# Performance work log

Hardware: AMD Instinct MI355X
Metric: run time of the kernel (lower is better)

Reference implementation:

```python
import jax, jax.numpy as jnp
import numpy as np

B, C, N = 8, 64, 4096

def setup_inputs() -> dict:
    key = jax.random.key(0)
    k1, k2, k3 = jax.random.split(key, 3)
    k = jax.random.normal(k1, (B, C, N), dtype=jnp.float32)
    q = jax.random.normal(k2, (B, C, N), dtype=jnp.float32)
    v = jax.random.normal(k3, (B, C, N), dtype=jnpp.float32) if False else jax.random.normal(k3, (B, C, N), dtype=jnp.float32)
    return {"k": k, "q": q, "v": v}

def reference(k, q, v):
    input_dim = k.shape[1]  # C
    # similarity = k^T @ q : [B, N, N]
    scores = jnp.einsum('bcn,bcm->bnm', k, q) / jnp.sqrt(jnp.float32(input_dim))
    attn = jax.nn.softmax(scores, axis=-1)  # softmax over last dim (query positions m)
    # out = attn @ v^T : [B, N, C], then transpose back to [B, C, N]
    out = jnp.einsum('bnm,bcm->bcn', attn, v)
    return out
```

## Files before the change

kernel.cpp:

```cpp
#include <hip/hip_runtime.h>
#include <stdint.h>

typedef __attribute__((ext_vector_type(8)))  __bf16        bf16x8;
typedef __attribute__((ext_vector_type(8)))  unsigned short u16x8;
typedef __attribute__((ext_vector_type(4)))  float          f32x4;
typedef __attribute__((ext_vector_type(16))) float          f32x16;
typedef __attribute__((ext_vector_type(4)))  unsigned int   u32x4;

#define NB 8
#define NC 64
#define NN 4096
#define NCHUNK 64
#define CHUNK_U16 4096
#define SPLITQ 4

#define EXP2F(x) __builtin_amdgcn_exp2f(x)

__device__ __forceinline__ unsigned short f2bf(float x) {
    unsigned int u = __builtin_bit_cast(unsigned int, x);
    u += 0x7fffu + ((u >> 16) & 1u);
    return (unsigned short)(u >> 16);
}
__device__ __forceinline__ unsigned int pk2(float a, float b) {
    unsigned short x = __builtin_bit_cast(unsigned short, (__bf16)a);
    unsigned short y = __builtin_bit_cast(unsigned short, (__bf16)b);
    return (unsigned int)x | ((unsigned int)y << 16);
}

__global__ __launch_bounds__(256) void prepass(
    const float* __restrict__ qp, const float* __restrict__ vp,
    unsigned short* __restrict__ qfo, unsigned short* __restrict__ vfo)
{
    __shared__ float lt[64][68];
    const int orig = blockIdx.x;
    const int bid = (orig & 7) * 64 + (orig >> 3);
    const int b = bid >> 6, mc = bid & 63;
    const int m0 = mc * 64;
    const int tid = threadIdx.x;
    const float* qb = qp + (size_t)b * NC * NN;
    const float* vb = vp + (size_t)b * NC * NN;
    unsigned short* qfc = qfo + (size_t)bid * CHUNK_U16;
    unsigned short* vfc = vfo + (size_t)bid * CHUNK_U16;

    #pragma unroll
    for (int rep = 0; rep < 4; ++rep) {
        int idx = tid + 256 * rep;
        int c = idx >> 4, m4 = (idx & 15) << 2;
        f32x4 xv = *reinterpret_cast<const f32x4*>(qb + (size_t)c * NN + m0 + m4);
        lt[m4+0][c] = xv[0]; lt[m4+1][c] = xv[1];
        lt[m4+2][c] = xv[2]; lt[m4+3][c] = xv[3];
    }
    __syncthreads();
    #pragma unroll
    for (int rep = 0; rep < 2; ++rep) {
        int fid = tid + 256 * rep;
        int l = fid & 63, kk = (fid >> 6) & 3, mt = fid >> 8;
        int m = 32 * mt + (l & 31), c0 = 16 * kk + 8 * (l >> 5);
        u16x8 ov;
        #pragma unroll
        for (int e = 0; e < 8; ++e) ov[e] = f2bf(lt[m][c0 + e]);
        *reinterpret_cast<u16x8*>(qfc + (size_t)fid * 8) = ov;
    }
    __syncthreads();
    #pragma unroll
    for (int rep = 0; rep < 4; ++rep) {
        int idx = tid + 256 * rep;
        int c = idx >> 4, m4 = (idx & 15) << 2;
        f32x4 xv = *reinterpret_cast<const f32x4*>(vb + (size_t)c * NN + m0 + m4);
        *reinterpret_cast<f32x4*>(&lt[c][m4]) = xv;
    }
    __syncthreads();
    #pragma unroll
    for (int rep = 0; rep < 2; ++rep) {
        int fid = tid + 256 * rep;
        int l = fid & 63, kt = (fid >> 6) & 3, ct = fid >> 8;
        int c = 32 * ct + (l & 31), mm = 16 * kt + 8 * (l >> 5);
        u16x8 ov;
        #pragma unroll
        for (int e = 0; e < 8; ++e) ov[e] = f2bf(lt[c][mm + e]);
        *reinterpret_cast<u16x8*>(vfc + (size_t)fid * 8) = ov;
    }
}

template<int SPLITQ_T>
__global__ __launch_bounds__(64, 3) void attn13(
    const float* __restrict__ kp,
    const unsigned short* __restrict__ qfo,
    const unsigned short* __restrict__ vfo,
    float* __restrict__ part, float* __restrict__ lp)
{
    constexpr int CPQ_T = NCHUNK / SPLITQ_T;
    constexpr int NT32 = NN / 32;
    constexpr int PER_XCD = SPLITQ_T * NT32;

    const int orig = blockIdx.x;
    const int bid  = (orig & 7) * PER_XCD + (orig >> 3);
    const int b    = bid / PER_XCD;
    const int rest = bid % PER_XCD;
    const int qid  = rest / NT32;
    const int t32  = rest % NT32;
    const int n0 = t32 * 32;
    const int l = threadIdx.x;
    const int lo5 = l & 31, hi = l >> 5;
    const int nrow = n0 + lo5;

    switch (orig & 3) {
        case 1: __builtin_amdgcn_s_sleep(5);  break;
        case 2: __builtin_amdgcn_s_sleep(10); break;
        case 3: __builtin_amdgcn_s_sleep(15); break;
        default: break;
    }

    const float kscale = 0.125f * 1.44269504088896f;
    const float* kb = kp + (size_t)b * NC * NN;
    bf16x8 kf[4];
    #pragma unroll
    for (int kk = 0; kk < 4; ++kk) {
        u16x8 t;
        #pragma unroll
        for (int e = 0; e < 8; ++e)
            t[e] = __builtin_bit_cast(unsigned short,
                      (__bf16)(kscale * kb[(size_t)(16 * kk + 8 * hi + e) * NN + nrow]));
        kf[kk] = __builtin_bit_cast(bf16x8, t);
    }

    const unsigned short* qg = qfo + (size_t)(b * NCHUNK + qid * CPQ_T) * CHUNK_U16;
    const unsigned short* vg = vfo + (size_t)(b * NCHUNK + qid * CPQ_T) * CHUNK_U16;

    f32x16 zro;
    #pragma unroll
    for (int r = 0; r < 16; ++r) zro[r] = 0.f;
    f32x16 o0 = zro, o1 = zro;
    float sum = 0.f;

    u16x8 a[8], vf[8];
    #pragma unroll
    for (int f = 0; f < 8; ++f)
        a[f] = *reinterpret_cast<const u16x8*>(qg + (f * 64 + l) * 8);
    #pragma unroll
    for (int f = 0; f < 8; ++f)
        vf[f] = *reinterpret_cast<const u16x8*>(vg + (f * 64 + l) * 8);

    for (int mcr = 0; mcr < CPQ_T; ++mcr) {
        __builtin_amdgcn_s_setprio(1);
        f32x16 s0 = __builtin_amdgcn_mfma_f32_32x32x16_bf16(__builtin_bit_cast(bf16x8, a[0]), kf[0], zro, 0, 0, 0);
        f32x16 s1 = __builtin_amdgcn_mfma_f32_32x32x16_bf16(__builtin_bit_cast(bf16x8, a[4]), kf[0], zro, 0, 0, 0);
        #pragma unroll
        for (int kk = 1; kk < 4; ++kk) {
            s0 = __builtin_amdgcn_mfma_f32_32x32x16_bf16(__builtin_bit_cast(bf16x8, a[kk]),     kf[kk], s0, 0, 0, 0);
            s1 = __builtin_amdgcn_mfma_f32_32x32x16_bf16(__builtin_bit_cast(bf16x8, a[4 + kk]), kf[kk], s1, 0, 0, 0);
        }
        __builtin_amdgcn_s_setprio(0);

        if (mcr + 1 < CPQ_T) {
            const unsigned short* qn = qg + (size_t)(mcr + 1) * CHUNK_U16;
            #pragma unroll
            for (int f = 0; f < 8; ++f)
                a[f] = *reinterpret_cast<const u16x8*>(qn + (f * 64 + l) * 8);
        }

        float ps0 = 0.f, ps1 = 0.f, ps2 = 0.f, ps3 = 0.f;
        #pragma unroll
        for (int r = 0; r < 16; r += 4) {
            s0[r]   = EXP2F(s0[r]);   ps0 += s0[r];
            s0[r+1] = EXP2F(s0[r+1]); ps1 += s0[r+1];
            s0[r+2] = EXP2F(s0[r+2]); ps2 += s0[r+2];
            s0[r+3] = EXP2F(s0[r+3]); ps3 += s0[r+3];
        }
        #pragma unroll
        for (int r = 0; r < 16; r += 4) {
            s1[r]   = EXP2F(s1[r]);   ps0 += s1[r];
            s1[r+1] = EXP2F(s1[r+1]); ps1 += s1[r+1];
            s1[r+2] = EXP2F(s1[r+2]); ps2 += s1[r+2];
            s1[r+3] = EXP2F(s1[r+3]); ps3 += s1[r+3];
        }
        sum += (ps0 + ps1) + (ps2 + ps3);

        #pragma unroll
        for (int kt = 0; kt < 4; ++kt) {
            const f32x16& sm = (kt < 2) ? s0 : s1;
            const int qA = 2 * (kt & 1);
            unsigned int w0 = pk2(sm[4*qA+0], sm[4*qA+1]);
            unsigned int w1 = pk2(sm[4*qA+2], sm[4*qA+3]);
            unsigned int w2 = pk2(sm[4*qA+4], sm[4*qA+5]);
            unsigned int w3 = pk2(sm[4*qA+6], sm[4*qA+7]);
            asm volatile("v_permlane32_swap_b32 %0, %1" : "+v"(w0), "+v"(w2));
            asm volatile("v_permlane32_swap_b32 %0, %1" : "+v"(w1), "+v"(w3));
            u32x4 pf = (u32x4){w0, w1, w2, w3};
            bf16x8 pB = __builtin_bit_cast(bf16x8, pf);
            __builtin_amdgcn_s_setprio(1);
            o0 = __builtin_amdgcn_mfma_f32_32x32x16_bf16(__builtin_bit_cast(bf16x8, vf[kt]),     pB, o0, 0, 0, 0);
            o1 = __builtin_amdgcn_mfma_f32_32x32x16_bf16(__builtin_bit_cast(bf16x8, vf[4 + kt]), pB, o1, 0, 0, 0);
            __builtin_amdgcn_s_setprio(0);
        }

        if (mcr + 1 < CPQ_T) {
            const unsigned short* vn = vg + (size_t)(mcr + 1) * CHUNK_U16;
            #pragma unroll
            for (int f = 0; f < 8; ++f)
                vf[f] = *reinterpret_cast<const u16x8*>(vn + (f * 64 + l) * 8);
        }
    }

    sum += (float)__shfl_xor(sum, 32);
    const int t64 = t32 >> 1;
    const int rowoff = 32 * (t32 & 1);
    const int pidx = (b * 64 + t64) * SPLITQ_T + qid;
    float* po = part + (size_t)pidx * 4096;
    #pragma unroll
    for (int r = 0; r < 16; ++r) {
        int cb = (r & 3) + 8 * (r >> 2) + 4 * hi;
        po[cb * 64 + rowoff + lo5]        = o0[r];
        po[(32 + cb) * 64 + rowoff + lo5] = o1[r];
    }
    if (hi == 0) lp[(size_t)pidx * 64 + rowoff + lo5] = sum;
}

__global__ __launch_bounds__(256) void combine2(
    const float* __restrict__ part, const float* __restrict__ lp,
    float* __restrict__ outp, int splitq)
{
    __shared__ float sinv[64];
    const int orig = blockIdx.x;
    const int bid = (orig & 7) * 64 + (orig >> 3);
    const int b = bid >> 6, tile = bid & 63;
    const int n0 = tile * 64;
    const int t = threadIdx.x;
    const int pb = bid * splitq;

    if (t < 64) {
        float L = 0.f;
        for (int q = 0; q < splitq; ++q) L += lp[(size_t)(pb + q) * 64 + t];
        sinv[t] = 1.0f / L;
    }
    __syncthreads();

    float* ob = outp + (size_t)b * NC * NN;
    #pragma unroll
    for (int it = 0; it < 4; ++it) {
        int idx = it * 1024 + t * 4;
        int ch = idx >> 6, r0 = idx & 63;
        f32x4 acc = (f32x4){0.f, 0.f, 0.f, 0.f};
        for (int q = 0; q < splitq; ++q) {
            f32x4 v = *reinterpret_cast<const f32x4*>(part + (size_t)(pb + q) * 4096 + idx);
            acc += v;
        }
        f32x4 res;
        #pragma unroll
        for (int u = 0; u < 4; ++u) res[u] = acc[u] * sinv[r0 + u];
        *reinterpret_cast<f32x4*>(ob + (size_t)ch * NN + n0 + r0) = res;
    }
}

__global__ __launch_bounds__(128) void attn2(
    const float* __restrict__ kp,
    const unsigned short* __restrict__ qfo,
    const unsigned short* __restrict__ vfo,
    float* __restrict__ outp)
{
    __shared__ unsigned short sb[2][2 * CHUNK_U16];
    const int orig = blockIdx.x;
    const int bid  = (orig & 7) * 64 + (orig >> 3);
    const int b = bid >> 6, nt = bid & 63;
    const int n0 = nt * 64;
    const int tid = threadIdx.x;
    const int w = tid >> 6, l = tid & 63;
    const int lo5 = l & 31, hi = l >> 5;
    const int nrow = n0 + 32 * w + lo5;
    const float kscale = 0.125f * 1.44269504088896f;
    const float* kb = kp + (size_t)b * NC * NN;
    bf16x8 kf[4];
    #pragma unroll
    for (int kk = 0; kk < 4; ++kk) {
        u16x8 t;
        #pragma unroll
        for (int e = 0; e < 8; ++e)
            t[e] = f2bf(kscale * kb[(size_t)(16 * kk + 8 * hi + e) * NN + nrow]);
        kf[kk] = __builtin_bit_cast(bf16x8, t);
    }
    const unsigned short* qg = qfo + (size_t)(b * 64) * CHUNK_U16;
    const unsigned short* vg = vfo + (size_t)(b * 64) * CHUNK_U16;
    auto stage = [&](int mc, int buf) {
        const unsigned short* gq = qg + (size_t)mc * CHUNK_U16;
        const unsigned short* gv = vg + (size_t)mc * CHUNK_U16;
        #pragma unroll
        for (int i = 0; i < 4; ++i) {
            int seg = w * 4 + i;
            int off = seg * 512 + l * 8;
            __builtin_amdgcn_global_load_lds(
                (const __attribute__((address_space(1))) void*)(gq + off),
                (__attribute__((address_space(3))) void*)(&sb[buf][seg * 512]), 16, 0, 0);
            __builtin_amdgcn_global_load_lds(
                (const __attribute__((address_space(1))) void*)(gv + off),
                (__attribute__((address_space(3))) void*)(&sb[buf][CHUNK_U16 + seg * 512]), 16, 0, 0);
        }
    };
    stage(0, 0);
    __syncthreads();
    f32x16 o0, o1;
    #pragma unroll
    for (int r = 0; r < 16; ++r) { o0[r] = 0.f; o1[r] = 0.f; }
    float m_run = -1e30f, l_run = 0.f;
    for (int mc = 0; mc < NCHUNK; ++mc) {
        const int cur = mc & 1;
        if (mc + 1 < NCHUNK) stage(mc + 1, cur ^ 1);
        const unsigned short* qb_ = &sb[cur][0];
        const unsigned short* vb_ = &sb[cur][CHUNK_U16];
        f32x16 s0, s1;
        #pragma unroll
        for (int r = 0; r < 16; ++r) { s0[r] = 0.f; s1[r] = 0.f; }
        #pragma unroll
        for (int kk = 0; kk < 4; ++kk) {
            u16x8 a0 = *reinterpret_cast<const u16x8*>(qb_ + ((0 * 4 + kk) * 64 + l) * 8);
            u16x8 a1 = *reinterpret_cast<const u16x8*>(qb_ + ((1 * 4 + kk) * 64 + l) * 8);
            s0 = __builtin_amdgcn_mfma_f32_32x32x16_bf16(__builtin_bit_cast(bf16x8, a0), kf[kk], s0, 0, 0, 0);
            s1 = __builtin_amdgcn_mfma_f32_32x32x16_bf16(__builtin_bit_cast(bf16x8, a1), kf[kk], s1, 0, 0, 0);
        }
        float pmax = s0[0];
        #pragma unroll
        for (int r = 1; r < 16; ++r) pmax = fmaxf(pmax, s0[r]);
        #pragma unroll
        for (int r = 0; r < 16; ++r) pmax = fmaxf(pmax, s1[r]);
        pmax = fmaxf(pmax, (float)__shfl_xor(pmax, 32));
        const float mn = fmaxf(m_run, pmax);
        const float alpha = EXP2F(m_run - mn);
        float sum = 0.f;
        #pragma unroll
        for (int r = 0; r < 16; ++r) { s0[r] = EXP2F(s0[r] - mn); sum += s0[r]; }
        #pragma unroll
        for (int r = 0; r < 16; ++r) { s1[r] = EXP2F(s1[r] - mn); sum += s1[r]; }
        sum += (float)__shfl_xor(sum, 32);
        l_run = l_run * alpha + sum;
        m_run = mn;
        #pragma unroll
        for (int r = 0; r < 16; ++r) { o0[r] *= alpha; o1[r] *= alpha; }
        #pragma unroll
        for (int kt = 0; kt < 4; ++kt) {
            const f32x16& sm = (kt < 2) ? s0 : s1;
            const int qA = 2 * (kt & 1);
            unsigned int dA0 = pk2(sm[4 * qA + 0], sm[4 * qA + 1]);
            unsigned int dA1 = pk2(sm[4 * qA + 2], sm[4 * qA + 3]);
            unsigned int dB0 = pk2(sm[4 * qA + 4], sm[4 * qA + 5]);
            unsigned int dB1 = pk2(sm[4 * qA + 6], sm[4 * qA + 7]);
            unsigned int sA0 = (unsigned int)__shfl_xor((int)dA0, 32);
            unsigned int sA1 = (unsigned int)__shfl_xor((int)dA1, 32);
            unsigned int sB0 = (unsigned int)__shfl_xor((int)dB0, 32);
            unsigned int sB1 = (unsigned int)__shfl_xor((int)dB1, 32);
            u32x4 pf;
            if (hi == 0) pf = (u32x4){dA0, dA1, sA0, sA1};
            else         pf = (u32x4){sB0, sB1, dB0, dB1};
            bf16x8 pB = __builtin_bit_cast(bf16x8, pf);
            u16x8 v0 = *reinterpret_cast<const u16x8*>(vb_ + ((0 * 4 + kt) * 64 + l) * 8);
            u16x8 v1 = *reinterpret_cast<const u16x8*>(vb_ + ((1 * 4 + kt) * 64 + l) * 8);
            o0 = __builtin_amdgcn_mfma_f32_32x32x16_bf16(__builtin_bit_cast(bf16x8, v0), pB, o0, 0, 0, 0);
            o1 = __builtin_amdgcn_mfma_f32_32x32x16_bf16(__builtin_bit_cast(bf16x8, v1), pB, o1, 0, 0, 0);
        }
        __syncthreads();
    }
    const float inv = 1.0f / l_run;
    float* ob = outp + (size_t)b * NC * NN;
    #pragma unroll
    for (int r = 0; r < 16; ++r) {
        int cb = (r & 3) + 8 * (r >> 2) + 4 * hi;
        ob[(size_t)cb * NN + n0 + 32 * w + lo5]        = o0[r] * inv;
        ob[(size_t)(32 + cb) * NN + n0 + 32 * w + lo5] = o1[r] * inv;
    }
}

__global__ __launch_bounds__(256) void attn_fwd(
    const float* __restrict__ kp, const float* __restrict__ qp,
    const float* __restrict__ vp, float* __restrict__ outp)
{
    __shared__ unsigned short qs[8][64][8];
    __shared__ unsigned short vs[8][64][8];
    __shared__ unsigned short ps[4][2][64][8];
    const int orig = blockIdx.x;
    const int bid  = (orig & 7) * 64 + (orig >> 3);
    const int b  = bid >> 6;
    const int n0 = (bid & 63) * 64;
    const int tid = threadIdx.x;
    const int w = tid >> 6, l = tid & 63, g = l >> 4, j = l & 15;
    const float* kb = kp + (size_t)b * NC * NN;
    const float* qb = qp + (size_t)b * NC * NN;
    const float* vb = vp + (size_t)b * NC * NN;
    bf16x8 ak[2];
    #pragma unroll
    for (int kk = 0; kk < 2; ++kk) {
        u16x8 tmp;
        #pragma unroll
        for (int e = 0; e < 8; ++e)
            tmp[e] = f2bf(kb[(size_t)(32*kk + 8*g + e) * NN + (n0 + 16*w + j)]);
        ak[kk] = __builtin_bit_cast(bf16x8, tmp);
    }
    f32x4 o[4];
    float m_run[4], l_run[4];
    #pragma unroll
    for (int ct = 0; ct < 4; ++ct) o[ct] = (f32x4){0.f,0.f,0.f,0.f};
    #pragma unroll
    for (int r = 0; r < 4; ++r) { m_run[r] = -1e30f; l_run[r] = 0.0f; }
    for (int m0 = 0; m0 < NN; m0 += 64) {
        __syncthreads();
        #pragma unroll
        for (int it = 0; it < 4; ++it) {
            int f = tid + 256*it;
            int c = f >> 4, m4 = (f & 15) << 2;
            f32x4 qv = *reinterpret_cast<const f32x4*>(qb + (size_t)c*NN + m0 + m4);
            f32x4 vv = *reinterpret_cast<const f32x4*>(vb + (size_t)c*NN + m0 + m4);
            int kkq = c >> 5, eq = c & 7, gq = (c >> 3) & 3, tq = m4 >> 4;
            #pragma unroll
            for (int u = 0; u < 4; ++u)
                qs[kkq*4 + tq][16*gq + ((m4 + u) & 15)][eq] = f2bf(qv[u]);
            int ctv = c >> 4, jv = c & 15, kkv = m4 >> 5, gv = (m4 >> 3) & 3, ev = m4 & 7;
            #pragma unroll
            for (int u = 0; u < 4; ++u)
                vs[kkv*4 + ctv][16*gv + jv][ev + u] = f2bf(vv[u]);
        }
        __syncthreads();
        f32x4 s[4];
        #pragma unroll
        for (int t = 0; t < 4; ++t) {
            f32x4 acc = (f32x4){0.f,0.f,0.f,0.f};
            #pragma unroll
            for (int kk = 0; kk < 2; ++kk) {
                u16x8 raw = *reinterpret_cast<const u16x8*>(&qs[kk*4 + t][l][0]);
                acc = __builtin_amdgcn_mfma_f32_16x16x32_bf16(ak[kk], __builtin_bit_cast(bf16x8, raw), acc, 0,0,0);
            }
            s[t] = acc * 0.125f;
        }
        float alpha[4];
        #pragma unroll
        for (int r = 0; r < 4; ++r) {
            float m1 = fmaxf(fmaxf(s[0][r], s[1][r]), fmaxf(s[2][r], s[3][r]));
            #pragma unroll
            for (int off = 1; off < 16; off <<= 1) m1 = fmaxf(m1, __shfl_xor(m1, off));
            float mn = fmaxf(m_run[r], m1);
            alpha[r] = __expf(m_run[r] - mn);
            m_run[r] = mn;
            float acc = 0.0f;
            #pragma unroll
            for (int t = 0; t < 4; ++t) { float p = __expf(s[t][r] - mn); s[t][r] = p; acc += p; }
            #pragma unroll
            for (int off = 1; off < 16; off <<= 1) acc += __shfl_xor(acc, off);
            l_run[r] = l_run[r] * alpha[r] + acc;
        }
        {
            int srcl = (j >> 2) << 4;
            float a0 = __shfl(alpha[0], srcl), a1 = __shfl(alpha[1], srcl);
            float a2 = __shfl(alpha[2], srcl), a3 = __shfl(alpha[3], srcl);
            int rs = j & 3;
            float ac = (rs==0)?a0:(rs==1)?a1:(rs==2)?a2:a3;
            #pragma unroll
            for (int ct = 0; ct < 4; ++ct) o[ct] *= ac;
        }
        #pragma unroll
        for (int t = 0; t < 4; ++t) {
            int m = 16*t + j;
            #pragma unroll
            for (int r = 0; r < 4; ++r)
                ps[w][m >> 5][((m >> 3) & 3)*16 + 4*g + r][m & 7] = f2bf(s[t][r]);
        }
        asm volatile("s_waitcnt lgkmcnt(0)" ::: "memory");
        #pragma unroll
        for (int kk2 = 0; kk2 < 2; ++kk2) {
            u16x8 rp = *reinterpret_cast<const u16x8*>(&ps[w][kk2][l][0]);
            bf16x8 bp = __builtin_bit_cast(bf16x8, rp);
            #pragma unroll
            for (int ct = 0; ct < 4; ++ct) {
                u16x8 rv = *reinterpret_cast<const u16x8*>(&vs[kk2*4 + ct][l][0]);
                o[ct] = __builtin_amdgcn_mfma_f32_16x16x32_bf16(__builtin_bit_cast(bf16x8, rv), bp, o[ct], 0,0,0);
            }
        }
    }
    {
        int srcl = (j >> 2) << 4;
        float l0 = __shfl(l_run[0], srcl), l1 = __shfl(l_run[1], srcl);
        float l2 = __shfl(l_run[2], srcl), l3 = __shfl(l_run[3], srcl);
        int rs = j & 3;
        float lc = (rs==0)?l0:(rs==1)?l1:(rs==2)?l2:l3;
        float inv = 1.0f / lc;
        #pragma unroll
        for (int ct = 0; ct < 4; ++ct)
            #pragma unroll
            for (int r = 0; r < 4; ++r)
                outp[(size_t)b*NC*NN + (size_t)(16*ct + 4*g + r)*NN + (n0 + 16*w + j)] = o[ct][r] * inv;
    }
}

extern "C" void kernel_launch(void* const* d_in, const int* in_sizes, int n_in,
                              void* d_out, int out_size, void* d_ws, size_t ws_size,
                              hipStream_t stream) {
    const float* kp = (const float*)d_in[0];
    const float* qp = (const float*)d_in[1];
    const float* vp = (const float*)d_in[2];
    float* op = (float*)d_out;
    const size_t FRAG_BYTES = (size_t)2 * NB * NCHUNK * CHUNK_U16 * sizeof(unsigned short);
    unsigned short* qfo = (unsigned short*)d_ws;
    unsigned short* vfo = qfo + (size_t)NB * NCHUNK * CHUNK_U16;

    const size_t NEED = FRAG_BYTES
        + (size_t)NB * 64 * SPLITQ * 4096 * sizeof(float)
        + (size_t)NB * 64 * SPLITQ * 64 * sizeof(float);

    if (ws_size >= NEED) {
        float* part = (float*)((char*)d_ws + FRAG_BYTES);
        float* lpp  = part + (size_t)NB * 64 * SPLITQ * 4096;
        hipLaunchKernelGGL(prepass, dim3(NB * NCHUNK), dim3(256), 0, stream, qp, vp, qfo, vfo);
        hipLaunchKernelGGL(attn13<SPLITQ>, dim3(NB * SPLITQ * (NN / 32)), dim3(64), 0, stream,
                           kp, qfo, vfo, part, lpp);
        hipLaunchKernelGGL(combine2, dim3(NB * 64), dim3(256), 0, stream, part, lpp, op, SPLITQ);
    } else if (ws_size >= FRAG_BYTES) {
        hipLaunchKernelGGL(prepass, dim3(NB * NCHUNK), dim3(256), 0, stream, qp, vp, qfo, vfo);
        hipLaunchKernelGGL(attn2, dim3(NB * NCHUNK), dim3(128), 0, stream, kp, qfo, vfo, op);
    } else {
        hipLaunchKernelGGL(attn_fwd, dim3(512), dim3(256), 0, stream, kp, qp, vp, op);
    }
}
```

Baseline: 70.21 us.

## Software-pipeline QK MFMA of next chunk with softmax of current chunk

Restructures the attention loop into a two-stage ping-pong: the QK^T MFMAs for chunk i+1 are issued while the exp and pack work for chunk i runs, with Q loads moved two chunks ahead. The goal is to overlap matrix-core latency with the VALU exponentials instead of running them back to back. It also drops the staggered s_sleep start, removes the setprio hints, and lowers the launch-bounds occupancy hint from 3 to 2 to leave room for the extra live score registers. Fewer waves per SIMD may reduce latency hiding across waves.

```diff
diff --git a/kernel.cpp b/kernel.cpp
--- a/kernel.cpp
+++ b/kernel.cpp
@@ -83,7 +83,7 @@
 }
 
 template<int SPLITQ_T>
-__global__ __launch_bounds__(64, 3) void attn13(
+__global__ __launch_bounds__(64, 2) void attn15(
     const float* __restrict__ kp,
     const unsigned short* __restrict__ qfo,
     const unsigned short* __restrict__ vfo,
@@ -104,13 +104,6 @@
     const int lo5 = l & 31, hi = l >> 5;
     const int nrow = n0 + lo5;
 
-    switch (orig & 3) {
-        case 1: __builtin_amdgcn_s_sleep(5);  break;
-        case 2: __builtin_amdgcn_s_sleep(10); break;
-        case 3: __builtin_amdgcn_s_sleep(15); break;
-        default: break;
-    }
-
     const float kscale = 0.125f * 1.44269504088896f;
     const float* kb = kp + (size_t)b * NC * NN;
     bf16x8 kf[4];
@@ -141,44 +134,40 @@
     for (int f = 0; f < 8; ++f)
         vf[f] = *reinterpret_cast<const u16x8*>(vg + (f * 64 + l) * 8);
 
-    for (int mcr = 0; mcr < CPQ_T; ++mcr) {
-        __builtin_amdgcn_s_setprio(1);
-        f32x16 s0 = __builtin_amdgcn_mfma_f32_32x32x16_bf16(__builtin_bit_cast(bf16x8, a[0]), kf[0], zro, 0, 0, 0);
-        f32x16 s1 = __builtin_amdgcn_mfma_f32_32x32x16_bf16(__builtin_bit_cast(bf16x8, a[4]), kf[0], zro, 0, 0, 0);
-        #pragma unroll
-        for (int kk = 1; kk < 4; ++kk) {
-            s0 = __builtin_amdgcn_mfma_f32_32x32x16_bf16(__builtin_bit_cast(bf16x8, a[kk]),     kf[kk], s0, 0, 0, 0);
-            s1 = __builtin_amdgcn_mfma_f32_32x32x16_bf16(__builtin_bit_cast(bf16x8, a[4 + kk]), kf[kk], s1, 0, 0, 0);
-        }
-        __builtin_amdgcn_s_setprio(0);
-
-        if (mcr + 1 < CPQ_T) {
-            const unsigned short* qn = qg + (size_t)(mcr + 1) * CHUNK_U16;
-            #pragma unroll
-            for (int f = 0; f < 8; ++f)
-                a[f] = *reinterpret_cast<const u16x8*>(qn + (f * 64 + l) * 8);
-        }
-
+    f32x16 sA0, sA1, sB0, sB1;
+    sA0 = __builtin_amdgcn_mfma_f32_32x32x16_bf16(__builtin_bit_cast(bf16x8, a[0]), kf[0], zro, 0, 0, 0);
+    sA1 = __builtin_amdgcn_mfma_f32_32x32x16_bf16(__builtin_bit_cast(bf16x8, a[4]), kf[0], zro, 0, 0, 0);
+    #pragma unroll
+    for (int kk = 1; kk < 4; ++kk) {
+        sA0 = __builtin_amdgcn_mfma_f32_32x32x16_bf16(__builtin_bit_cast(bf16x8, a[kk]),     kf[kk], sA0, 0, 0, 0);
+        sA1 = __builtin_amdgcn_mfma_f32_32x32x16_bf16(__builtin_bit_cast(bf16x8, a[4 + kk]), kf[kk], sA1, 0, 0, 0);
+    }
+    #pragma unroll
+    for (int f = 0; f < 8; ++f)
+        a[f] = *reinterpret_cast<const u16x8*>(qg + CHUNK_U16 + (f * 64 + l) * 8);
+
+    auto phase = [&](f32x16& c0, f32x16& c1, f32x16& nx0, f32x16& nx1, int idx) {
         float ps0 = 0.f, ps1 = 0.f, ps2 = 0.f, ps3 = 0.f;
         #pragma unroll
         for (int r = 0; r < 16; r += 4) {
-            s0[r]   = EXP2F(s0[r]);   ps0 += s0[r];
-            s0[r+1] = EXP2F(s0[r+1]); ps1 += s0[r+1];
-            s0[r+2] = EXP2F(s0[r+2]); ps2 += s0[r+2];
-            s0[r+3] = EXP2F(s0[r+3]); ps3 += s0[r+3];
+            c0[r]   = EXP2F(c0[r]);   ps0 += c0[r];
+            c0[r+1] = EXP2F(c0[r+1]); ps1 += c0[r+1];
+            c0[r+2] = EXP2F(c0[r+2]); ps2 += c0[r+2];
+            c0[r+3] = EXP2F(c0[r+3]); ps3 += c0[r+3];
         }
         #pragma unroll
         for (int r = 0; r < 16; r += 4) {
-            s1[r]   = EXP2F(s1[r]);   ps0 += s1[r];
-            s1[r+1] = EXP2F(s1[r+1]); ps1 += s1[r+1];
-            s1[r+2] = EXP2F(s1[r+2]); ps2 += s1[r+2];
-            s1[r+3] = EXP2F(s1[r+3]); ps3 += s1[r+3];
+            c1[r]   = EXP2F(c1[r]);   ps0 += c1[r];
+            c1[r+1] = EXP2F(c1[r+1]); ps1 += c1[r+1];
+            c1[r+2] = EXP2F(c1[r+2]); ps2 += c1[r+2];
+            c1[r+3] = EXP2F(c1[r+3]); ps3 += c1[r+3];
         }
         sum += (ps0 + ps1) + (ps2 + ps3);
 
+        bf16x8 pB[4];
         #pragma unroll
         for (int kt = 0; kt < 4; ++kt) {
-            const f32x16& sm = (kt < 2) ? s0 : s1;
+            const f32x16& sm = (kt < 2) ? c0 : c1;
             const int qA = 2 * (kt & 1);
             unsigned int w0 = pk2(sm[4*qA+0], sm[4*qA+1]);
             unsigned int w1 = pk2(sm[4*qA+2], sm[4*qA+3]);
@@ -187,19 +176,41 @@
             asm volatile("v_permlane32_swap_b32 %0, %1" : "+v"(w0), "+v"(w2));
             asm volatile("v_permlane32_swap_b32 %0, %1" : "+v"(w1), "+v"(w3));
             u32x4 pf = (u32x4){w0, w1, w2, w3};
-            bf16x8 pB = __builtin_bit_cast(bf16x8, pf);
-            __builtin_amdgcn_s_setprio(1);
-            o0 = __builtin_amdgcn_mfma_f32_32x32x16_bf16(__builtin_bit_cast(bf16x8, vf[kt]),     pB, o0, 0, 0, 0);
-            o1 = __builtin_amdgcn_mfma_f32_32x32x16_bf16(__builtin_bit_cast(bf16x8, vf[4 + kt]), pB, o1, 0, 0, 0);
-            __builtin_amdgcn_s_setprio(0);
-        }
-
-        if (mcr + 1 < CPQ_T) {
-            const unsigned short* vn = vg + (size_t)(mcr + 1) * CHUNK_U16;
+            pB[kt] = __builtin_bit_cast(bf16x8, pf);
+        }
+
+        if (idx + 1 < CPQ_T) {
+            nx0 = __builtin_amdgcn_mfma_f32_32x32x16_bf16(__builtin_bit_cast(bf16x8, a[0]), kf[0], zro, 0, 0, 0);
+            nx1 = __builtin_amdgcn_mfma_f32_32x32x16_bf16(__builtin_bit_cast(bf16x8, a[4]), kf[0], zro, 0, 0, 0);
+            #pragma unroll
+            for (int kk = 1; kk < 4; ++kk) {
+                nx0 = __builtin_amdgcn_mfma_f32_32x32x16_bf16(__builtin_bit_cast(bf16x8, a[kk]),     kf[kk], nx0, 0, 0, 0);
+                nx1 = __builtin_amdgcn_mfma_f32_32x32x16_bf16(__builtin_bit_cast(bf16x8, a[4 + kk]), kf[kk], nx1, 0, 0, 0);
+            }
+        }
+        if (idx + 2 < CPQ_T) {
+            const unsigned short* qn = qg + (size_t)(idx + 2) * CHUNK_U16;
+            #pragma unroll
+            for (int f = 0; f < 8; ++f)
+                a[f] = *reinterpret_cast<const u16x8*>(qn + (f * 64 + l) * 8);
+        }
+
+        #pragma unroll
+        for (int kt = 0; kt < 4; ++kt) {
+            o0 = __builtin_amdgcn_mfma_f32_32x32x16_bf16(__builtin_bit_cast(bf16x8, vf[kt]),     pB[kt], o0, 0, 0, 0);
+            o1 = __builtin_amdgcn_mfma_f32_32x32x16_bf16(__builtin_bit_cast(bf16x8, vf[4 + kt]), pB[kt], o1, 0, 0, 0);
+        }
+        if (idx + 1 < CPQ_T) {
+            const unsigned short* vn = vg + (size_t)(idx + 1) * CHUNK_U16;
             #pragma unroll
             for (int f = 0; f < 8; ++f)
                 vf[f] = *reinterpret_cast<const u16x8*>(vn + (f * 64 + l) * 8);
         }
+    };
+
+    for (int i = 0; i < CPQ_T; i += 2) {
+        phase(sA0, sA1, sB0, sB1, i);
+        phase(sB0, sB1, sA0, sA1, i + 1);
     }
 
     sum += (float)__shfl_xor(sum, 32);
@@ -505,7 +516,7 @@
         float* part = (float*)((char*)d_ws + FRAG_BYTES);
         float* lpp  = part + (size_t)NB * 64 * SPLITQ * 4096;
         hipLaunchKernelGGL(prepass, dim3(NB * NCHUNK), dim3(256), 0, stream, qp, vp, qfo, vfo);
-        hipLaunchKernelGGL(attn13<SPLITQ>, dim3(NB * SPLITQ * (NN / 32)), dim3(64), 0, stream,
+        hipLaunchKernelGGL(attn15<SPLITQ>, dim3(NB * SPLITQ * (NN / 32)), dim3(64), 0, stream,
                            kp, qfo, vfo, part, lpp);
         hipLaunchKernelGGL(combine2, dim3(NB * 64), dim3(256), 0, stream, part, lpp, op, SPLITQ);
     } else if (ws_size >= FRAG_BYTES) {
```

Result: no change. 70.34 us (+0.2%).
